# Kernel tuning notes

Measured on AMD Instinct MI355X. Metric: run time of the kernel, lower is better.

Reference implementation:

```python
import jax, jax.numpy as jnp
import numpy as np


def setup_inputs() -> dict:
    key = jax.random.key(0)
    k1, k2 = jax.random.split(key)
    recon_points = jax.random.normal(k1, (4, 4096, 3), dtype=jnp.float32)
    gt_points = jax.random.normal(k2, (4, 4096, 3), dtype=jnp.float32)
    return {"recon_points": recon_points, "gt_points": gt_points}


def reference(recon_points, gt_points):
    # Pairwise squared distances: [B, N, M]
    diff = recon_points[:, :, None, :] - gt_points[:, None, :, :]  # [B,N,M,D]
    dist = jnp.sum(diff * diff, axis=3)                            # [B,N,M]
    dist_min1 = jnp.min(dist, axis=2)  # nearest gt for each recon point [B,N]
    dist_min2 = jnp.min(dist, axis=1)  # nearest recon for each gt point [B,M]
    loss = (jnp.mean(dist_min1) + jnp.mean(dist_min2)) / 2
    return loss
```

## Files before the change

### kernel.cpp

```cpp
#include <hip/hip_runtime.h>

#define CD_B 4
#define CD_N 4096
#define CD_M 4096
#define TILE 256

__global__ __launch_bounds__(256) void cd_init(uint4* __restrict__ mins,
                                               float* __restrict__ out) {
    if (blockIdx.x == 0 && threadIdx.x == 0) out[0] = 0.f;
    const unsigned int inf = 0x7F800000u;
    mins[blockIdx.x * 256 + threadIdx.x] = make_uint4(inf, inf, inf, inf);
}

__global__ __launch_bounds__(256, 4) void cd_main(const float* __restrict__ recon,
                                                  const float* __restrict__ gt,
                                                  unsigned int* __restrict__ rmin,
                                                  unsigned int* __restrict__ cmin) {
    const int bid = blockIdx.x;
    const int b   = bid >> 8;
    const int ti  = (bid >> 4) & 15;
    const int tj  = bid & 15;
    const int t   = threadIdx.x;
    const int w   = t >> 6;
    const int l   = t & 63;

    __shared__ float4 rs[TILE];
    __shared__ float4 gs[TILE];
    __shared__ float  part[4][TILE];

    {
        const float* rp = recon + ((size_t)(b * CD_N + ti * TILE) + t) * 3;
        const float* gp = gt    + ((size_t)(b * CD_M + tj * TILE) + t) * 3;
        const float rx = rp[0], ry = rp[1], rz = rp[2];
        const float gx = gp[0], gy = gp[1], gz = gp[2];
        rs[t] = make_float4(rx, ry, rz, fmaf(rz, rz, fmaf(ry, ry, rx * rx)));
        gs[t] = make_float4(gx, gy, gz, fmaf(gz, gz, fmaf(gy, gy, gx * gx)));
    }
    __syncthreads();

    const float INF = __builtin_inff();

    {
        const float4 p0 = rs[l], p1 = rs[64 + l], p2 = rs[128 + l], p3 = rs[192 + l];
        const float a0x = -2.f * p0.x, a0y = -2.f * p0.y, a0z = -2.f * p0.z;
        const float a1x = -2.f * p1.x, a1y = -2.f * p1.y, a1z = -2.f * p1.z;
        const float a2x = -2.f * p2.x, a2y = -2.f * p2.y, a2z = -2.f * p2.z;
        const float a3x = -2.f * p3.x, a3y = -2.f * p3.y, a3z = -2.f * p3.z;
        float m0 = INF, m1 = INF, m2 = INF, m3 = INF;
        const int jbase = w << 6;
        #pragma unroll 8
        for (int jj = 0; jj < 64; jj += 2) {
            const float4 g0 = gs[jbase + jj];
            const float4 g1 = gs[jbase + jj + 1];
            float d0, d1;
            d0 = fmaf(a0x, g0.x, fmaf(a0y, g0.y, fmaf(a0z, g0.z, g0.w)));
            d1 = fmaf(a0x, g1.x, fmaf(a0y, g1.y, fmaf(a0z, g1.z, g1.w)));
            m0 = fminf(fminf(d0, d1), m0);
            d0 = fmaf(a1x, g0.x, fmaf(a1y, g0.y, fmaf(a1z, g0.z, g0.w)));
            d1 = fmaf(a1x, g1.x, fmaf(a1y, g1.y, fmaf(a1z, g1.z, g1.w)));
            m1 = fminf(fminf(d0, d1), m1);
            d0 = fmaf(a2x, g0.x, fmaf(a2y, g0.y, fmaf(a2z, g0.z, g0.w)));
            d1 = fmaf(a2x, g1.x, fmaf(a2y, g1.y, fmaf(a2z, g1.z, g1.w)));
            m2 = fminf(fminf(d0, d1), m2);
            d0 = fmaf(a3x, g0.x, fmaf(a3y, g0.y, fmaf(a3z, g0.z, g0.w)));
            d1 = fmaf(a3x, g1.x, fmaf(a3y, g1.y, fmaf(a3z, g1.z, g1.w)));
            m3 = fminf(fminf(d0, d1), m3);
        }
        part[w][l]       = m0;
        part[w][64 + l]  = m1;
        part[w][128 + l] = m2;
        part[w][192 + l] = m3;
    }
    __syncthreads();
    {
        const float v = fminf(fminf(part[0][t], part[1][t]),
                              fminf(part[2][t], part[3][t]));
        const float dist = fmaxf(v + rs[t].w, 0.f);
        atomicMin(&rmin[b * CD_N + ti * TILE + t], __float_as_uint(dist));
    }
    __syncthreads();

    {
        const float4 q0 = gs[l], q1 = gs[64 + l], q2 = gs[128 + l], q3 = gs[192 + l];
        const float a0x = -2.f * q0.x, a0y = -2.f * q0.y, a0z = -2.f * q0.z;
        const float a1x = -2.f * q1.x, a1y = -2.f * q1.y, a1z = -2.f * q1.z;
        const float a2x = -2.f * q2.x, a2y = -2.f * q2.y, a2z = -2.f * q2.z;
        const float a3x = -2.f * q3.x, a3y = -2.f * q3.y, a3z = -2.f * q3.z;
        float m0 = INF, m1 = INF, m2 = INF, m3 = INF;
        const int ibase = w << 6;
        #pragma unroll 8
        for (int ii = 0; ii < 64; ii += 2) {
            const float4 r0 = rs[ibase + ii];
            const float4 r1 = rs[ibase + ii + 1];
            float d0, d1;
            d0 = fmaf(a0x, r0.x, fmaf(a0y, r0.y, fmaf(a0z, r0.z, r0.w)));
            d1 = fmaf(a0x, r1.x, fmaf(a0y, r1.y, fmaf(a0z, r1.z, r1.w)));
            m0 = fminf(fminf(d0, d1), m0);
            d0 = fmaf(a1x, r0.x, fmaf(a1y, r0.y, fmaf(a1z, r0.z, r0.w)));
            d1 = fmaf(a1x, r1.x, fmaf(a1y, r1.y, fmaf(a1z, r1.z, r1.w)));
            m1 = fminf(fminf(d0, d1), m1);
            d0 = fmaf(a2x, r0.x, fmaf(a2y, r0.y, fmaf(a2z, r0.z, r0.w)));
            d1 = fmaf(a2x, r1.x, fmaf(a2y, r1.y, fmaf(a2z, r1.z, r1.w)));
            m2 = fminf(fminf(d0, d1), m2);
            d0 = fmaf(a3x, r0.x, fmaf(a3y, r0.y, fmaf(a3z, r0.z, r0.w)));
            d1 = fmaf(a3x, r1.x, fmaf(a3y, r1.y, fmaf(a3z, r1.z, r1.w)));
            m3 = fminf(fminf(d0, d1), m3);
        }
        part[w][l]       = m0;
        part[w][64 + l]  = m1;
        part[w][128 + l] = m2;
        part[w][192 + l] = m3;
    }
    __syncthreads();
    {
        const float v = fminf(fminf(part[0][t], part[1][t]),
                              fminf(part[2][t], part[3][t]));
        const float dist = fmaxf(v + gs[t].w, 0.f);
        atomicMin(&cmin[b * CD_M + tj * TILE + t], __float_as_uint(dist));
    }
}

__global__ __launch_bounds__(256) void cd_reduce(const unsigned int* __restrict__ mins,
                                                 float* __restrict__ out) {
    const int total = CD_B * (CD_N + CD_M);
    float s = 0.f;
    for (int i = blockIdx.x * 256 + threadIdx.x; i < total; i += 64 * 256)
        s += __uint_as_float(mins[i]);
    for (int off = 32; off; off >>= 1) s += __shfl_down(s, off);
    __shared__ float ws[4];
    const int t = threadIdx.x;
    if ((t & 63) == 0) ws[t >> 6] = s;
    __syncthreads();
    if (t == 0) {
        const float tot = ws[0] + ws[1] + ws[2] + ws[3];
        atomicAdd(out, tot * (0.5f / (float)(CD_B * CD_N)));
    }
}

extern "C" void kernel_launch(void* const* d_in, const int* in_sizes, int n_in,
                              void* d_out, int out_size, void* d_ws, size_t ws_size,
                              hipStream_t stream) {
    const float* recon = (const float*)d_in[0];
    const float* gt    = (const float*)d_in[1];
    unsigned int* rmin = (unsigned int*)d_ws;
    unsigned int* cmin = rmin + CD_B * CD_N;
    float* out = (float*)d_out;

    cd_init<<<32, 256, 0, stream>>>((uint4*)rmin, out);
    cd_main<<<CD_B * 16 * 16, 256, 0, stream>>>(recon, gt, rmin, cmin);
    cd_reduce<<<64, 256, 0, stream>>>(rmin, out);
}
```

Baseline: 68.15 us.

## Stream wave-uniform point lists per own-point, drop atomicMin workspace and reduce kernel

Replaces the tiled shared-memory scheme with a prep kernel that packs both point clouds into float4 (xyz plus squared norm). The main kernel then has each thread own one point and each wave scan 1024 points of the other cloud straight from global memory, using a wave-uniform index so the loads can be scalar/broadcast. Per-block minima are combined in LDS and summed straight into the output with one atomicAdd per block. This removes the init and reduce launches and the global atomicMin traffic. In exchange each thread keeps only one accumulator, so there is less register-level reuse, and grid parallelism drops to 512 blocks.

```diff
diff --git a/kernel.cpp b/kernel.cpp
--- a/kernel.cpp
+++ b/kernel.cpp
@@ -1,139 +1,62 @@
 #include <hip/hip_runtime.h>
 
 #define CD_B 4
-#define CD_N 4096
-#define CD_M 4096
-#define TILE 256
+#define CD_NPTS 4096
+#define CD_TOTAL (CD_B * CD_NPTS)
 
-__global__ __launch_bounds__(256) void cd_init(uint4* __restrict__ mins,
+__global__ __launch_bounds__(256) void cd_prep(const float* __restrict__ recon,
+                                               const float* __restrict__ gt,
+                                               float4* __restrict__ pts4,
                                                float* __restrict__ out) {
-    if (blockIdx.x == 0 && threadIdx.x == 0) out[0] = 0.f;
-    const unsigned int inf = 0x7F800000u;
-    mins[blockIdx.x * 256 + threadIdx.x] = make_uint4(inf, inf, inf, inf);
+    const int i = blockIdx.x * 256 + threadIdx.x;
+    if (i == 0) out[0] = 0.f;
+    const int idx = i & (CD_TOTAL - 1);
+    const float* src = (i < CD_TOTAL) ? recon : gt;
+    const float x = src[idx * 3 + 0];
+    const float y = src[idx * 3 + 1];
+    const float z = src[idx * 3 + 2];
+    pts4[i] = make_float4(x, y, z, fmaf(z, z, fmaf(y, y, x * x)));
 }
 
-__global__ __launch_bounds__(256, 4) void cd_main(const float* __restrict__ recon,
-                                                  const float* __restrict__ gt,
-                                                  unsigned int* __restrict__ rmin,
-                                                  unsigned int* __restrict__ cmin) {
+__global__ __launch_bounds__(256) void cd_main(const float4* __restrict__ pts4,
+                                               float* __restrict__ out) {
     const int bid = blockIdx.x;
-    const int b   = bid >> 8;
-    const int ti  = (bid >> 4) & 15;
-    const int tj  = bid & 15;
+    const int dir = bid >> 8;
+    const int b   = (bid >> 6) & 3;
+    const int pg  = bid & 63;
     const int t   = threadIdx.x;
-    const int w   = t >> 6;
     const int l   = t & 63;
+    const int w   = __builtin_amdgcn_readfirstlane(t >> 6);
 
-    __shared__ float4 rs[TILE];
-    __shared__ float4 gs[TILE];
-    __shared__ float  part[4][TILE];
+    const float4* rs4 = pts4;
+    const float4* gs4 = pts4 + CD_TOTAL;
+    const float4* own    = (dir == 0 ? rs4 : gs4) + b * CD_NPTS + pg * 64;
+    const float4* stream = (dir == 0 ? gs4 : rs4) + b * CD_NPTS + w * 1024;
 
-    {
-        const float* rp = recon + ((size_t)(b * CD_N + ti * TILE) + t) * 3;
-        const float* gp = gt    + ((size_t)(b * CD_M + tj * TILE) + t) * 3;
-        const float rx = rp[0], ry = rp[1], rz = rp[2];
-        const float gx = gp[0], gy = gp[1], gz = gp[2];
-        rs[t] = make_float4(rx, ry, rz, fmaf(rz, rz, fmaf(ry, ry, rx * rx)));
-        gs[t] = make_float4(gx, gy, gz, fmaf(gz, gz, fmaf(gy, gy, gx * gx)));
+    const float4 p = own[l];
+    const float ax = -2.f * p.x, ay = -2.f * p.y, az = -2.f * p.z;
+
+    float m = __builtin_inff();
+    #pragma unroll 4
+    for (int j = 0; j < 1024; j += 2) {
+        const float4 g0 = stream[j];
+        const float4 g1 = stream[j + 1];
+        const float d0 = fmaf(ax, g0.x, fmaf(ay, g0.y, fmaf(az, g0.z, g0.w)));
+        const float d1 = fmaf(ax, g1.x, fmaf(ay, g1.y, fmaf(az, g1.z, g1.w)));
+        m = fminf(fminf(d0, d1), m);
     }
+
+    __shared__ float part[4][64];
+    part[w][l] = m;
     __syncthreads();
 
-    const float INF = __builtin_inff();
-
-    {
-        const float4 p0 = rs[l], p1 = rs[64 + l], p2 = rs[128 + l], p3 = rs[192 + l];
-        const float a0x = -2.f * p0.x, a0y = -2.f * p0.y, a0z = -2.f * p0.z;
-        const float a1x = -2.f * p1.x, a1y = -2.f * p1.y, a1z = -2.f * p1.z;
-        const float a2x = -2.f * p2.x, a2y = -2.f * p2.y, a2z = -2.f * p2.z;
-        const float a3x = -2.f * p3.x, a3y = -2.f * p3.y, a3z = -2.f * p3.z;
-        float m0 = INF, m1 = INF, m2 = INF, m3 = INF;
-        const int jbase = w << 6;
-        #pragma unroll 8
-        for (int jj = 0; jj < 64; jj += 2) {
-            const float4 g0 = gs[jbase + jj];
-            const float4 g1 = gs[jbase + jj + 1];
-            float d0, d1;
-            d0 = fmaf(a0x, g0.x, fmaf(a0y, g0.y, fmaf(a0z, g0.z, g0.w)));
-            d1 = fmaf(a0x, g1.x, fmaf(a0y, g1.y, fmaf(a0z, g1.z, g1.w)));
-            m0 = fminf(fminf(d0, d1), m0);
-            d0 = fmaf(a1x, g0.x, fmaf(a1y, g0.y, fmaf(a1z, g0.z, g0.w)));
-            d1 = fmaf(a1x, g1.x, fmaf(a1y, g1.y, fmaf(a1z, g1.z, g1.w)));
-            m1 = fminf(fminf(d0, d1), m1);
-            d0 = fmaf(a2x, g0.x, fmaf(a2y, g0.y, fmaf(a2z, g0.z, g0.w)));
-            d1 = fmaf(a2x, g1.x, fmaf(a2y, g1.y, fmaf(a2z, g1.z, g1.w)));
-            m2 = fminf(fminf(d0, d1), m2);
-            d0 = fmaf(a3x, g0.x, fmaf(a3y, g0.y, fmaf(a3z, g0.z, g0.w)));
-            d1 = fmaf(a3x, g1.x, fmaf(a3y, g1.y, fmaf(a3z, g1.z, g1.w)));
-            m3 = fminf(fminf(d0, d1), m3);
-        }
-        part[w][l]       = m0;
-        part[w][64 + l]  = m1;
-        part[w][128 + l] = m2;
-        part[w][192 + l] = m3;
-    }
-    __syncthreads();
-    {
-        const float v = fminf(fminf(part[0][t], part[1][t]),
-                              fminf(part[2][t], part[3][t]));
-        const float dist = fmaxf(v + rs[t].w, 0.f);
-        atomicMin(&rmin[b * CD_N + ti * TILE + t], __float_as_uint(dist));
-    }
-    __syncthreads();
-
-    {
-        const float4 q0 = gs[l], q1 = gs[64 + l], q2 = gs[128 + l], q3 = gs[192 + l];
-        const float a0x = -2.f * q0.x, a0y = -2.f * q0.y, a0z = -2.f * q0.z;
-        const float a1x = -2.f * q1.x, a1y = -2.f * q1.y, a1z = -2.f * q1.z;
-        const float a2x = -2.f * q2.x, a2y = -2.f * q2.y, a2z = -2.f * q2.z;
-        const float a3x = -2.f * q3.x, a3y = -2.f * q3.y, a3z = -2.f * q3.z;
-        float m0 = INF, m1 = INF, m2 = INF, m3 = INF;
-        const int ibase = w << 6;
-        #pragma unroll 8
-        for (int ii = 0; ii < 64; ii += 2) {
-            const float4 r0 = rs[ibase + ii];
-            const float4 r1 = rs[ibase + ii + 1];
-            float d0, d1;
-            d0 = fmaf(a0x, r0.x, fmaf(a0y, r0.y, fmaf(a0z, r0.z, r0.w)));
-            d1 = fmaf(a0x, r1.x, fmaf(a0y, r1.y, fmaf(a0z, r1.z, r1.w)));
-            m0 = fminf(fminf(d0, d1), m0);
-            d0 = fmaf(a1x, r0.x, fmaf(a1y, r0.y, fmaf(a1z, r0.z, r0.w)));
-            d1 = fmaf(a1x, r1.x, fmaf(a1y, r1.y, fmaf(a1z, r1.z, r1.w)));
-            m1 = fminf(fminf(d0, d1), m1);
-            d0 = fmaf(a2x, r0.x, fmaf(a2y, r0.y, fmaf(a2z, r0.z, r0.w)));
-            d1 = fmaf(a2x, r1.x, fmaf(a2y, r1.y, fmaf(a2z, r1.z, r1.w)));
-            m2 = fminf(fminf(d0, d1), m2);
-            d0 = fmaf(a3x, r0.x, fmaf(a3y, r0.y, fmaf(a3z, r0.z, r0.w)));
-            d1 = fmaf(a3x, r1.x, fmaf(a3y, r1.y, fmaf(a3z, r1.z, r1.w)));
-            m3 = fminf(fminf(d0, d1), m3);
-        }
-        part[w][l]       = m0;
-        part[w][64 + l]  = m1;
-        part[w][128 + l] = m2;
-        part[w][192 + l] = m3;
-    }
-    __syncthreads();
-    {
-        const float v = fminf(fminf(part[0][t], part[1][t]),
-                              fminf(part[2][t], part[3][t]));
-        const float dist = fmaxf(v + gs[t].w, 0.f);
-        atomicMin(&cmin[b * CD_M + tj * TILE + t], __float_as_uint(dist));
-    }
-}
-
-__global__ __launch_bounds__(256) void cd_reduce(const unsigned int* __restrict__ mins,
-                                                 float* __restrict__ out) {
-    const int total = CD_B * (CD_N + CD_M);
-    float s = 0.f;
-    for (int i = blockIdx.x * 256 + threadIdx.x; i < total; i += 64 * 256)
-        s += __uint_as_float(mins[i]);
-    for (int off = 32; off; off >>= 1) s += __shfl_down(s, off);
-    __shared__ float ws[4];
-    const int t = threadIdx.x;
-    if ((t & 63) == 0) ws[t >> 6] = s;
-    __syncthreads();
-    if (t == 0) {
-        const float tot = ws[0] + ws[1] + ws[2] + ws[3];
-        atomicAdd(out, tot * (0.5f / (float)(CD_B * CD_N)));
+    if (w == 0) {
+        float v = fminf(fminf(part[0][l], part[1][l]),
+                        fminf(part[2][l], part[3][l]));
+        v = fmaxf(v + p.w, 0.f);
+        for (int off = 32; off; off >>= 1) v += __shfl_down(v, off);
+        if (l == 0)
+            atomicAdd(out, v * (0.5f / (float)CD_TOTAL));
     }
 }
 
@@ -142,11 +65,9 @@
                               hipStream_t stream) {
     const float* recon = (const float*)d_in[0];
     const float* gt    = (const float*)d_in[1];
-    unsigned int* rmin = (unsigned int*)d_ws;
-    unsigned int* cmin = rmin + CD_B * CD_N;
+    float4* pts4 = (float4*)d_ws;
     float* out = (float*)d_out;
 
-    cd_init<<<32, 256, 0, stream>>>((uint4*)rmin, out);
-    cd_main<<<CD_B * 16 * 16, 256, 0, stream>>>(recon, gt, rmin, cmin);
-    cd_reduce<<<64, 256, 0, stream>>>(rmin, out);
+    cd_prep<<<128, 256, 0, stream>>>(recon, gt, pts4, out);
+    cd_main<<<512, 256, 0, stream>>>(pts4, out);
 }
```

After: 142.0 us. 108% more time.

## Replace atomicMin accumulation with per-tile partial minima and gather kernel

Applied to the files above, without the earlier changes.

The main kernel now writes each tile's row and column minima to a workspace buffer of partial results instead of issuing global atomicMin. A new gather kernel takes the min over the 16 partial tiles per point and sums. This removes the init kernel launch and the atomic contention, and folds the output zeroing into the tile kernel. In exchange it writes and reads a 2 MB workspace, and the output reset now relies on the tile kernel finishing before the gather kernel's atomicAdds.

```diff
diff --git a/kernel.cpp b/kernel.cpp
--- a/kernel.cpp
+++ b/kernel.cpp
@@ -2,20 +2,13 @@
 
 #define CD_B 4
 #define CD_N 4096
-#define CD_M 4096
+#define CD_TOTAL (CD_B * CD_N)
 #define TILE 256
 
-__global__ __launch_bounds__(256) void cd_init(uint4* __restrict__ mins,
-                                               float* __restrict__ out) {
-    if (blockIdx.x == 0 && threadIdx.x == 0) out[0] = 0.f;
-    const unsigned int inf = 0x7F800000u;
-    mins[blockIdx.x * 256 + threadIdx.x] = make_uint4(inf, inf, inf, inf);
-}
-
-__global__ __launch_bounds__(256, 4) void cd_main(const float* __restrict__ recon,
-                                                  const float* __restrict__ gt,
-                                                  unsigned int* __restrict__ rmin,
-                                                  unsigned int* __restrict__ cmin) {
+__global__ __launch_bounds__(256, 4) void cd_tiles(const float* __restrict__ recon,
+                                                   const float* __restrict__ gt,
+                                                   float* __restrict__ pm,
+                                                   float* __restrict__ out) {
     const int bid = blockIdx.x;
     const int b   = bid >> 8;
     const int ti  = (bid >> 4) & 15;
@@ -24,13 +17,15 @@
     const int w   = t >> 6;
     const int l   = t & 63;
 
+    if (bid == 0 && t == 0) out[0] = 0.f;
+
     __shared__ float4 rs[TILE];
     __shared__ float4 gs[TILE];
     __shared__ float  part[4][TILE];
 
     {
         const float* rp = recon + ((size_t)(b * CD_N + ti * TILE) + t) * 3;
-        const float* gp = gt    + ((size_t)(b * CD_M + tj * TILE) + t) * 3;
+        const float* gp = gt    + ((size_t)(b * CD_N + tj * TILE) + t) * 3;
         const float rx = rp[0], ry = rp[1], rz = rp[2];
         const float gx = gp[0], gy = gp[1], gz = gp[2];
         rs[t] = make_float4(rx, ry, rz, fmaf(rz, rz, fmaf(ry, ry, rx * rx)));
@@ -76,7 +71,7 @@
         const float v = fminf(fminf(part[0][t], part[1][t]),
                               fminf(part[2][t], part[3][t]));
         const float dist = fmaxf(v + rs[t].w, 0.f);
-        atomicMin(&rmin[b * CD_N + ti * TILE + t], __float_as_uint(dist));
+        pm[(((b << 4) + ti) << 12) + (tj << 8) + t] = dist;
     }
     __syncthreads();
 
@@ -116,24 +111,30 @@
         const float v = fminf(fminf(part[0][t], part[1][t]),
                               fminf(part[2][t], part[3][t]));
         const float dist = fmaxf(v + gs[t].w, 0.f);
-        atomicMin(&cmin[b * CD_M + tj * TILE + t], __float_as_uint(dist));
+        pm[262144 + (((b << 4) + tj) << 12) + (ti << 8) + t] = dist;
     }
 }
 
-__global__ __launch_bounds__(256) void cd_reduce(const unsigned int* __restrict__ mins,
+__global__ __launch_bounds__(256) void cd_gather(const float* __restrict__ pm,
                                                  float* __restrict__ out) {
-    const int total = CD_B * (CD_N + CD_M);
-    float s = 0.f;
-    for (int i = blockIdx.x * 256 + threadIdx.x; i < total; i += 64 * 256)
-        s += __uint_as_float(mins[i]);
-    for (int off = 32; off; off >>= 1) s += __shfl_down(s, off);
+    const int tid = blockIdx.x * 256 + threadIdx.x;
+    const int p   = tid & 255;
+    const int ot  = (tid >> 8) & 15;
+    const int gb  = tid >> 12;
+    const float* base = pm + ((((gb << 4) + ot) << 4) << 8) + p;
+
+    float m = base[0];
+    #pragma unroll
+    for (int st = 1; st < 16; ++st) m = fminf(m, base[st << 8]);
+
+    for (int off = 32; off; off >>= 1) m += __shfl_down(m, off);
     __shared__ float ws[4];
     const int t = threadIdx.x;
-    if ((t & 63) == 0) ws[t >> 6] = s;
+    if ((t & 63) == 0) ws[t >> 6] = m;
     __syncthreads();
     if (t == 0) {
-        const float tot = ws[0] + ws[1] + ws[2] + ws[3];
-        atomicAdd(out, tot * (0.5f / (float)(CD_B * CD_N)));
+        const float s = ws[0] + ws[1] + ws[2] + ws[3];
+        atomicAdd(out, s * (0.5f / (float)CD_TOTAL));
     }
 }
 
@@ -142,11 +143,9 @@
                               hipStream_t stream) {
     const float* recon = (const float*)d_in[0];
     const float* gt    = (const float*)d_in[1];
-    unsigned int* rmin = (unsigned int*)d_ws;
-    unsigned int* cmin = rmin + CD_B * CD_N;
+    float* pm  = (float*)d_ws;
     float* out = (float*)d_out;
 
-    cd_init<<<32, 256, 0, stream>>>((uint4*)rmin, out);
-    cd_main<<<CD_B * 16 * 16, 256, 0, stream>>>(recon, gt, rmin, cmin);
-    cd_reduce<<<64, 256, 0, stream>>>(rmin, out);
+    cd_tiles<<<CD_B * 16 * 16, 256, 0, stream>>>(recon, gt, pm, out);
+    cd_gather<<<128, 256, 0, stream>>>(pm, out);
 }
```

Result: no change. 68.60 us (+0.7%).
